# Optimization experiments

Measured on AMD Instinct MI355X. Metric: run time of the kernel, lower is better.

## Reference

```python
import jax, jax.numpy as jnp
import numpy as np
from jax import lax


def setup_inputs() -> dict:
    key = jax.random.key(0)
    I = jax.random.uniform(key, (32, 3, 512, 512), dtype=jnp.float32)
    return {"I": I, "k": 15}


def reference(I, k):
    # Channel-wise min -> dark channel (torch does this via -max_pool over transposed channel dim)
    dark = jnp.min(I, axis=1, keepdims=True)  # [B,1,H,W]
    p = k // 2
    # Spatial min-pool kxk, stride 1, pad k//2. torch max_pool2d pads with -inf,
    # so the min-pool equivalent pads with +inf: reduce_window with min and +inf init.
    eroded = lax.reduce_window(
        dark,
        jnp.inf,
        lax.min,
        window_dimensions=(1, 1, k, k),
        window_strides=(1, 1, 1, 1),
        padding=[(0, 0), (0, 0), (p, p), (p, p)],
    )
    return eroded
```

## Files before the change

kernel.cpp:

```cpp
#include <hip/hip_runtime.h>
#include <math.h>

#define BATCH 32
#define CH    3
#define H     512
#define W     512
#define KWIN  15
#define PAD   7
#define TH    8

__global__ __launch_bounds__(256, 8) void dcp_fused2(const float* __restrict__ I,
                                                     float* __restrict__ out) {
    const int b  = blockIdx.y;
    const int y0 = blockIdx.x * TH;
    const int t  = threadIdx.x;
    const int x  = t * 2;

    __shared__ float tile[TH][W + 2 * PAD + 2];

    const float* base = I + (size_t)b * CH * H * W;

    auto load_cm = [&](int y) -> float2 {
        float2 r;
        if (y < 0 || y >= H) { r.x = INFINITY; r.y = INFINITY; return r; }
        const float2 a0 = *(const float2*)(base + ((size_t)0 * H + y) * W + x);
        const float2 a1 = *(const float2*)(base + ((size_t)1 * H + y) * W + x);
        const float2 a2 = *(const float2*)(base + ((size_t)2 * H + y) * W + x);
        r.x = fminf(fminf(a0.x, a1.x), a2.x);
        r.y = fminf(fminf(a0.y, a1.y), a2.y);
        return r;
    };

    float2 P[PAD];
    {
        float2 run = load_cm(y0 + 8);
        P[0] = run;
        #pragma unroll
        for (int k = 1; k < PAD; ++k) {
            const float2 c = load_cm(y0 + 8 + k);
            run.x = fminf(run.x, c.x); run.y = fminf(run.y, c.y);
            P[k] = run;
        }
    }
    float2 U = load_cm(y0 + 7);
    #pragma unroll
    for (int i = 13; i >= 8; --i) {
        const float2 c = load_cm(y0 - PAD + i);
        U.x = fminf(U.x, c.x); U.y = fminf(U.y, c.y);
    }
    #pragma unroll
    for (int i = PAD; i >= 0; --i) {
        const float2 c = load_cm(y0 - PAD + i);
        U.x = fminf(U.x, c.x); U.y = fminf(U.y, c.y);
        float2 o;
        if (i > 0) { o.x = fminf(U.x, P[i - 1].x); o.y = fminf(U.y, P[i - 1].y); }
        else       { o = U; }
        *(float2*)&tile[i][PAD + x] = o;
    }

    if (t < PAD) {
        #pragma unroll
        for (int r = 0; r < TH; ++r) tile[r][t] = INFINITY;
    } else if (t < 2 * PAD) {
        #pragma unroll
        for (int r = 0; r < TH; ++r) tile[r][W + t] = INFINITY;
    }
    __syncthreads();

    #pragma unroll
    for (int r = 0; r < TH; ++r) {
        float2 w[8];
        #pragma unroll
        for (int j = 0; j < 8; ++j) w[j] = *(const float2*)&tile[r][x + 2 * j];
        float m = fminf(w[0].y, w[7].x);
        #pragma unroll
        for (int j = 1; j < 7; ++j) m = fminf(m, fminf(w[j].x, w[j].y));
        float2 o;
        o.x = fminf(m, w[0].x);
        o.y = fminf(m, w[7].y);
        *(float2*)(out + ((size_t)b * H + y0 + r) * W + x) = o;
    }
}

extern "C" void kernel_launch(void* const* d_in, const int* in_sizes, int n_in,
                              void* d_out, int out_size, void* d_ws, size_t ws_size,
                              hipStream_t stream) {
    const float* I = (const float*)d_in[0];
    float* out = (float*)d_out;
    dcp_fused2<<<dim3(H / TH, BATCH), dim3(256), 0, stream>>>(I, out);
}
```

Before: 176.4 us.

## Widen to float4 per thread and batch all channel loads up front

Each thread now covers four columns using float4 loads, with 128 threads per block. All 22 halo rows for each channel are loaded into registers ahead of time using clamped row indices, with no per-row branching, and out-of-range rows are masked to infinity only in the edge blocks. The horizontal min over the shared tile is rebuilt around a shared interior minimum for the four outputs. The aim is more memory-level parallelism and wider transactions, at the cost of heavy register use (22 float4 values) and fewer threads per block.

```diff
diff --git a/kernel.cpp b/kernel.cpp
--- a/kernel.cpp
+++ b/kernel.cpp
@@ -8,77 +8,94 @@
 #define KWIN  15
 #define PAD   7
 #define TH    8
+#define NR    (TH + KWIN - 1)
 
-__global__ __launch_bounds__(256, 8) void dcp_fused2(const float* __restrict__ I,
+static __device__ __forceinline__ float4 min4(float4 a, float4 b) {
+    float4 r;
+    r.x = fminf(a.x, b.x); r.y = fminf(a.y, b.y);
+    r.z = fminf(a.z, b.z); r.w = fminf(a.w, b.w);
+    return r;
+}
+
+__global__ __launch_bounds__(128, 3) void dcp_fused3(const float* __restrict__ I,
                                                      float* __restrict__ out) {
     const int b  = blockIdx.y;
     const int y0 = blockIdx.x * TH;
     const int t  = threadIdx.x;
-    const int x  = t * 2;
+    const int x  = t * 4;
 
-    __shared__ float tile[TH][W + 2 * PAD + 2];
+    __shared__ float tile[TH][W + 16];
 
     const float* base = I + (size_t)b * CH * H * W;
 
-    auto load_cm = [&](int y) -> float2 {
-        float2 r;
-        if (y < 0 || y >= H) { r.x = INFINITY; r.y = INFINITY; return r; }
-        const float2 a0 = *(const float2*)(base + ((size_t)0 * H + y) * W + x);
-        const float2 a1 = *(const float2*)(base + ((size_t)1 * H + y) * W + x);
-        const float2 a2 = *(const float2*)(base + ((size_t)2 * H + y) * W + x);
-        r.x = fminf(fminf(a0.x, a1.x), a2.x);
-        r.y = fminf(fminf(a0.y, a1.y), a2.y);
-        return r;
-    };
+    float4 v[NR];
 
-    float2 P[PAD];
-    {
-        float2 run = load_cm(y0 + 8);
-        P[0] = run;
+    #pragma unroll
+    for (int i = 0; i < NR; ++i) {
+        const int y = min(max(y0 - PAD + i, 0), H - 1);
+        v[i] = *(const float4*)(base + ((size_t)0 * H + y) * W + x);
+    }
+    #pragma unroll
+    for (int i = 0; i < NR; ++i) {
+        const int y = min(max(y0 - PAD + i, 0), H - 1);
+        const float4 c = *(const float4*)(base + ((size_t)1 * H + y) * W + x);
+        v[i] = min4(v[i], c);
+    }
+    #pragma unroll
+    for (int i = 0; i < NR; ++i) {
+        const int y = min(max(y0 - PAD + i, 0), H - 1);
+        const float4 c = *(const float4*)(base + ((size_t)2 * H + y) * W + x);
+        v[i] = min4(v[i], c);
+    }
+    if (blockIdx.x == 0 || blockIdx.x == gridDim.x - 1) {
+        const float4 inf4 = make_float4(INFINITY, INFINITY, INFINITY, INFINITY);
         #pragma unroll
-        for (int k = 1; k < PAD; ++k) {
-            const float2 c = load_cm(y0 + 8 + k);
-            run.x = fminf(run.x, c.x); run.y = fminf(run.y, c.y);
-            P[k] = run;
+        for (int i = 0; i < NR; ++i) {
+            const int y = y0 - PAD + i;
+            if (y < 0 || y >= H) v[i] = inf4;
         }
     }
-    float2 U = load_cm(y0 + 7);
+
+    float4 P[PAD];
+    P[0] = v[15];
     #pragma unroll
-    for (int i = 13; i >= 8; --i) {
-        const float2 c = load_cm(y0 - PAD + i);
-        U.x = fminf(U.x, c.x); U.y = fminf(U.y, c.y);
-    }
+    for (int k = 1; k < PAD; ++k) P[k] = min4(P[k - 1], v[15 + k]);
+    float4 U = v[14];
+    #pragma unroll
+    for (int i = 13; i >= 8; --i) U = min4(U, v[i]);
     #pragma unroll
     for (int i = PAD; i >= 0; --i) {
-        const float2 c = load_cm(y0 - PAD + i);
-        U.x = fminf(U.x, c.x); U.y = fminf(U.y, c.y);
-        float2 o;
-        if (i > 0) { o.x = fminf(U.x, P[i - 1].x); o.y = fminf(U.y, P[i - 1].y); }
-        else       { o = U; }
-        *(float2*)&tile[i][PAD + x] = o;
+        U = min4(U, v[i]);
+        const float4 o = (i > 0) ? min4(U, P[i - 1]) : U;
+        *(float4*)&tile[i][8 + x] = o;
     }
 
-    if (t < PAD) {
-        #pragma unroll
-        for (int r = 0; r < TH; ++r) tile[r][t] = INFINITY;
-    } else if (t < 2 * PAD) {
-        #pragma unroll
-        for (int r = 0; r < TH; ++r) tile[r][W + t] = INFINITY;
+    if (t < 64) {
+        const int r = t >> 3, c = t & 7;
+        tile[r][c]           = INFINITY;
+        tile[r][8 + W + c]   = INFINITY;
     }
     __syncthreads();
 
     #pragma unroll
     for (int r = 0; r < TH; ++r) {
-        float2 w[8];
-        #pragma unroll
-        for (int j = 0; j < 8; ++j) w[j] = *(const float2*)&tile[r][x + 2 * j];
-        float m = fminf(w[0].y, w[7].x);
-        #pragma unroll
-        for (int j = 1; j < 7; ++j) m = fminf(m, fminf(w[j].x, w[j].y));
-        float2 o;
-        o.x = fminf(m, w[0].x);
-        o.y = fminf(m, w[7].y);
-        *(float2*)(out + ((size_t)b * H + y0 + r) * W + x) = o;
+        float4 w0 = *(const float4*)&tile[r][x];
+        float4 w1 = *(const float4*)&tile[r][x + 4];
+        float4 w2 = *(const float4*)&tile[r][x + 8];
+        float4 w3 = *(const float4*)&tile[r][x + 12];
+        float4 w4 = *(const float4*)&tile[r][x + 16];
+        float4 q = min4(min4(w1, w2), w3);
+        const float common = fminf(fminf(q.x, q.y), fminf(q.z, q.w));
+        const float a   = fminf(w0.z, w0.w);
+        const float L0  = fminf(w0.y, a);
+        const float r01 = fminf(w4.x, w4.y);
+        const float r012= fminf(r01, w4.z);
+        float4 o;
+        o.x = fminf(common, L0);
+        o.y = fminf(fminf(common, a), w4.x);
+        o.z = fminf(fminf(common, w0.w), r01);
+        o.w = fminf(common, r012);
+        *(float4*)(out + ((size_t)b * H + y0 + r) * W + x) = o;
     }
 }
 
@@ -87,5 +104,5 @@
                               hipStream_t stream) {
     const float* I = (const float*)d_in[0];
     float* out = (float*)d_out;
-    dcp_fused2<<<dim3(H / TH, BATCH), dim3(256), 0, stream>>>(I, out);
+    dcp_fused3<<<dim3(H / TH, BATCH), dim3(128), 0, stream>>>(I, out);
 }
```

After: 210.2 us. 1.19x slower.
